# Kernel optimization log

Measured on AMD Instinct MI355X. Metric: run time of the kernel, lower is better.

The kernel has to match this reference:

```python
import jax, jax.numpy as jnp
import numpy as np

B, S, H, D = 4, 2048, 16, 64

def setup_inputs() -> dict:
    key = jax.random.key(0)
    kq, kk, kv = jax.random.split(key, 3)
    q = jax.random.normal(kq, (B, S, H, D), dtype=jnp.float32)
    k = jax.random.normal(kk, (B, S, H, D), dtype=jnp.float32)
    v = jax.random.normal(kv, (B, S, H, D), dtype=jnp.float32)
    return {"q": q, "k": k, "v": v}

def reference(q, k, v):
    # q,k,v: [B,S,H,D]; mask=None path -> additive causal mask; training=False (no dropout)
    batch, seq_len, num_heads, head_dim = q.shape
    scale = head_dim ** -0.5
    qk = jnp.einsum('bqhd,bkhd->bhqk', q, k) * scale  # [B,H,S,S]
    causal = jnp.triu(jnp.ones((seq_len, seq_len), dtype=qk.dtype), k=1)  # 1 above diagonal
    qk = qk + causal[None, None] * jnp.asarray(-1e9, dtype=qk.dtype)
    attn = jax.nn.softmax(qk, axis=-1)
    out = jnp.einsum('bhqk,bkhd->bqhd', attn, v)  # [B,S,H,D]
    return out
```

## Files before the change

### kernel.cpp

```cpp
#include <hip/hip_runtime.h>

#define S_  2048
#define H_  16
#define D_  64
#define HD_ (H_ * D_)
#define LDP 40

using bf16x8 = __attribute__((ext_vector_type(8))) __bf16;
using bf16x4 = __attribute__((ext_vector_type(4))) __bf16;
using f32x4  = __attribute__((ext_vector_type(4))) float;

__device__ __forceinline__ f32x4 mfma16(bf16x8 a, bf16x8 b, f32x4 c) {
    return __builtin_amdgcn_mfma_f32_16x16x32_bf16(a, b, c, 0, 0, 0);
}

__device__ __forceinline__ void glds16(const void* g, void* l) {
    __builtin_amdgcn_global_load_lds((const __attribute__((address_space(1))) void*)g,
                                     (__attribute__((address_space(3))) void*)l, 16, 0, 0);
}

__global__ __launch_bounds__(256, 4)
void prepack(const float* __restrict__ Kg, const float* __restrict__ Vg,
             __bf16* __restrict__ Kb, __bf16* __restrict__ Vtb) {
    __shared__ __bf16 T[64 * 66];
    const int tid = threadIdx.x;
    const int st  = blockIdx.x;
    const int bh  = blockIdx.y;
    const int b = bh >> 4, h = bh & 15;
    if (blockIdx.z == 0) {
#pragma unroll
        for (int rep = 0; rep < 4; ++rep) {
            int lin = rep * 256 + tid;
            int r  = lin >> 4;
            int dq = (lin & 15) << 2;
            float4 x = *(const float4*)(Kg + ((size_t)(b * S_ + st * 64 + r) * H_ + h) * D_ + dq);
            bf16x4 u = {(__bf16)x.x, (__bf16)x.y, (__bf16)x.z, (__bf16)x.w};
            *(bf16x4*)(Kb + ((size_t)bh * S_ + st * 64 + r) * D_ + dq) = u;
        }
    } else {
#pragma unroll
        for (int rep = 0; rep < 4; ++rep) {
            int lin = rep * 256 + tid;
            int r  = lin >> 4;
            int dq = (lin & 15) << 2;
            float4 x = *(const float4*)(Vg + ((size_t)(b * S_ + st * 64 + r) * H_ + h) * D_ + dq);
            T[r * 66 + dq + 0] = (__bf16)x.x;
            T[r * 66 + dq + 1] = (__bf16)x.y;
            T[r * 66 + dq + 2] = (__bf16)x.z;
            T[r * 66 + dq + 3] = (__bf16)x.w;
        }
        __syncthreads();
#pragma unroll
        for (int rep = 0; rep < 4; ++rep) {
            int lin = rep * 256 + tid;
            int d  = lin >> 4;
            int s4 = (lin & 15) << 2;
            bf16x4 u = {T[(s4 + 0) * 66 + d], T[(s4 + 1) * 66 + d],
                        T[(s4 + 2) * 66 + d], T[(s4 + 3) * 66 + d]};
            *(bf16x4*)(Vtb + ((size_t)bh * D_ + d) * S_ + st * 64 + s4) = u;
        }
    }
}

__global__ __launch_bounds__(256, 4)
void fa_fwd(const float* __restrict__ Qg,
            const __bf16* __restrict__ Kb, const __bf16* __restrict__ Vtb,
            float* __restrict__ Og) {
    __shared__ __align__(16) __bf16 Kbuf[2][2048];
    __shared__ __align__(16) __bf16 Vbuf[2][2048];
    __shared__ __bf16 Ps[2560];

    const int tid  = threadIdx.x;
    const int lane = tid & 63;
    const int wave = tid >> 6;
    const int l16  = lane & 15;
    const int quad = lane >> 4;

    const int p   = blockIdx.x;
    const int tHi = 31 - p;
    const int tLo = p;
    const int bh  = blockIdx.y;
    const int b   = bh >> 4;
    const int h   = bh & 15;

    const float sc = 0.18033688f;

    const int kl = lane >> 3, ksl = lane & 7;
    const __bf16* kdma = Kb + ((size_t)bh * S_ + wave * 8 + kl) * D_ + ((ksl ^ kl) << 3);
    const int dl = lane >> 2, vsl = lane & 3;
    const __bf16* vdma = Vtb + ((size_t)bh * D_ + wave * 16 + dl) * S_ + ((vsl ^ (dl & 3)) << 3);

    glds16(kdma, &Kbuf[0][wave * 512]);
    glds16(vdma, &Vbuf[0][wave * 512]);

    const size_t qbase = (size_t)b * S_ * HD_ + (size_t)h * D_;
    const float* Qp = Qg + qbase;
    float*       Op = Og + qbase;
    bf16x8 qh[2], ql[2];
#pragma unroll
    for (int kf = 0; kf < 2; ++kf) {
        const float* qph = Qp + (size_t)(tHi * 64 + wave * 16 + l16) * HD_ + quad * 8 + kf * 32;
        const float* qpl = Qp + (size_t)(tLo * 64 + wave * 16 + l16) * HD_ + quad * 8 + kf * 32;
        float4 x = *(const float4*)(qph);
        float4 y = *(const float4*)(qph + 4);
        bf16x8 f;
        f[0] = (__bf16)x.x; f[1] = (__bf16)x.y; f[2] = (__bf16)x.z; f[3] = (__bf16)x.w;
        f[4] = (__bf16)y.x; f[5] = (__bf16)y.y; f[6] = (__bf16)y.z; f[7] = (__bf16)y.w;
        qh[kf] = f;
        x = *(const float4*)(qpl);
        y = *(const float4*)(qpl + 4);
        f[0] = (__bf16)x.x; f[1] = (__bf16)x.y; f[2] = (__bf16)x.z; f[3] = (__bf16)x.w;
        f[4] = (__bf16)y.x; f[5] = (__bf16)y.y; f[6] = (__bf16)y.z; f[7] = (__bf16)y.w;
        ql[kf] = f;
    }

    f32x4 oh[4], ol[4];
    float lh[4], ll[4];
#pragma unroll
    for (int nd = 0; nd < 4; ++nd) { oh[nd] = (f32x4)0.f; ol[nd] = (f32x4)0.f; }
#pragma unroll
    for (int r = 0; r < 4; ++r) { lh[r] = 0.f; ll[r] = 0.f; }

    auto process = [&](f32x4* s, bool diag, int dOff, f32x4* oacc, float* lsum, int cb) {
#pragma unroll
        for (int nt = 0; nt < 2; ++nt)
#pragma unroll
            for (int r = 0; r < 4; ++r) {
                float v = s[nt][r] * sc;
                if (diag && (dOff + nt * 16 + l16 > wave * 16 + quad * 4 + r)) v = -1e30f;
                float pe = __builtin_amdgcn_exp2f(v);
                s[nt][r] = pe;
                lsum[r] += pe;
            }
        __bf16* pw = &Ps[(wave * 16 + quad * 4) * LDP + l16];
#pragma unroll
        for (int r = 0; r < 4; ++r)
#pragma unroll
            for (int nt = 0; nt < 2; ++nt)
                pw[r * LDP + nt * 16] = (__bf16)s[nt][r];
        bf16x8 a = *(const bf16x8*)&Ps[(wave * 16 + l16) * LDP + quad * 8];
#pragma unroll
        for (int nd = 0; nd < 4; ++nd) {
            bf16x8 bv = *(const bf16x8*)&Vbuf[cb][(nd * 16 + l16) * 32 + ((quad ^ (l16 & 3)) << 3)];
            oacc[nd] = mfma16(a, bv, oacc[nd]);
        }
    };

    const int nkt = 64 - 2 * p;
    __syncthreads();
    for (int kt = 0; kt < nkt; ++kt) {
        const int cb = kt & 1;
        if (kt + 1 < nkt) {
            glds16(kdma + (size_t)(kt + 1) * 2048, &Kbuf[cb ^ 1][wave * 512]);
            glds16(vdma + (kt + 1) * 32,           &Vbuf[cb ^ 1][wave * 512]);
        }
        const bool loAct = (kt < 2 * p + 2);
        f32x4 sh[2], sl[2];
#pragma unroll
        for (int nt = 0; nt < 2; ++nt) { sh[nt] = (f32x4)0.f; sl[nt] = (f32x4)0.f; }
#pragma unroll
        for (int nt = 0; nt < 2; ++nt)
#pragma unroll
            for (int kf = 0; kf < 2; ++kf) {
                bf16x8 bk = *(const bf16x8*)&Kbuf[cb][(nt * 16 + l16) * 64 +
                                 ((((kf << 2) + quad) ^ (l16 & 7)) << 3)];
                sh[nt] = mfma16(qh[kf], bk, sh[nt]);
                if (loAct) sl[nt] = mfma16(ql[kf], bk, sl[nt]);
            }
        process(sh, kt >= 2 * tHi, kt * 32 - tHi * 64, oh, lh, cb);
        if (loAct) process(sl, kt >= 2 * tLo, kt * 32 - tLo * 64, ol, ll, cb);
        __syncthreads();
    }

    auto finish = [&](f32x4* oacc, float* lsum, int trow) {
#pragma unroll
        for (int r = 0; r < 4; ++r) {
            float s = lsum[r];
            s += __shfl_xor(s, 1);
            s += __shfl_xor(s, 2);
            s += __shfl_xor(s, 4);
            s += __shfl_xor(s, 8);
            float inv = 1.0f / s;
            float* op = Op + (size_t)(trow * 64 + wave * 16 + quad * 4 + r) * HD_;
#pragma unroll
            for (int nd = 0; nd < 4; ++nd)
                op[nd * 16 + l16] = oacc[nd][r] * inv;
        }
    };
    finish(oh, lh, tHi);
    finish(ol, ll, tLo);
}

#define LDAF 66
#define LDPF 68
__global__ __launch_bounds__(256, 4)
void fa_fwd_fb(const float* __restrict__ Qg, const float* __restrict__ Kg,
               const float* __restrict__ Vg, float* __restrict__ Og) {
    __shared__ __bf16 Ks[64 * LDAF];
    __shared__ __bf16 Vt[64 * LDAF];
    __shared__ __bf16 Ps[4 * 16 * LDPF];
    const int tid = threadIdx.x, lane = tid & 63, wave = tid >> 6;
    const int l16 = lane & 15, quad = lane >> 4;
    const int p = blockIdx.x, tHi = 31 - p, tLo = p;
    const int bh = blockIdx.y, b = bh >> 4, h = bh & 15;
    const float sc = 0.18033688f;
    const size_t base = (size_t)b * S_ * HD_ + (size_t)h * D_;
    const float* Qp = Qg + base; const float* Kp = Kg + base;
    const float* Vp = Vg + base; float* Op = Og + base;
    bf16x8 qh[2], ql[2];
#pragma unroll
    for (int kf = 0; kf < 2; ++kf) {
        const float* qph = Qp + (size_t)(tHi * 64 + wave * 16 + l16) * HD_ + quad * 8 + kf * 32;
        const float* qpl = Qp + (size_t)(tLo * 64 + wave * 16 + l16) * HD_ + quad * 8 + kf * 32;
        float4 x = *(const float4*)(qph); float4 y = *(const float4*)(qph + 4);
        bf16x8 f;
        f[0]=(__bf16)x.x; f[1]=(__bf16)x.y; f[2]=(__bf16)x.z; f[3]=(__bf16)x.w;
        f[4]=(__bf16)y.x; f[5]=(__bf16)y.y; f[6]=(__bf16)y.z; f[7]=(__bf16)y.w;
        qh[kf] = f;
        x = *(const float4*)(qpl); y = *(const float4*)(qpl + 4);
        f[0]=(__bf16)x.x; f[1]=(__bf16)x.y; f[2]=(__bf16)x.z; f[3]=(__bf16)x.w;
        f[4]=(__bf16)y.x; f[5]=(__bf16)y.y; f[6]=(__bf16)y.z; f[7]=(__bf16)y.w;
        ql[kf] = f;
    }
    f32x4 oh[4], ol[4]; float lh[4], ll[4];
#pragma unroll
    for (int nd = 0; nd < 4; ++nd) { oh[nd] = (f32x4)0.f; ol[nd] = (f32x4)0.f; }
#pragma unroll
    for (int r = 0; r < 4; ++r) { lh[r] = 0.f; ll[r] = 0.f; }
    auto process = [&](f32x4* s, bool diag, f32x4* oacc, float* lsum) {
#pragma unroll
        for (int nt = 0; nt < 4; ++nt)
#pragma unroll
            for (int r = 0; r < 4; ++r) {
                float v = s[nt][r] * sc;
                if (diag && (nt * 16 + l16 > wave * 16 + quad * 4 + r)) v = -1e30f;
                float pe = __builtin_amdgcn_exp2f(v);
                s[nt][r] = pe; lsum[r] += pe;
            }
        __bf16* pw = &Ps[(wave * 16 + quad * 4) * LDPF + l16];
#pragma unroll
        for (int r = 0; r < 4; ++r)
#pragma unroll
            for (int nt = 0; nt < 4; ++nt) pw[r * LDPF + nt * 16] = (__bf16)s[nt][r];
        const __bf16* pr = &Ps[wave * 16 * LDPF];
#pragma unroll
        for (int kf = 0; kf < 2; ++kf) {
            bf16x8 a = *(const bf16x8*)&pr[l16 * LDPF + kf * 32 + quad * 8];
#pragma unroll
            for (int nd = 0; nd < 4; ++nd) {
                bf16x8 bv = *(const bf16x8*)&Vt[(nd * 16 + l16) * LDAF + kf * 32 + quad * 8];
                oacc[nd] = mfma16(a, bv, oacc[nd]);
            }
        }
    };
    const int nkt = 32 - p;
    for (int kt = 0; kt < nkt; ++kt) {
        __syncthreads();
#pragma unroll
        for (int rep = 0; rep < 4; ++rep) {
            int linear = rep * 256 + tid;
            int key = linear >> 4; int dq = (linear & 15) << 2;
            const float* kp = Kp + (size_t)(kt * 64 + key) * HD_ + dq;
            const float* vp = Vp + (size_t)(kt * 64 + key) * HD_ + dq;
            float4 kv = *(const float4*)kp; float4 vv = *(const float4*)vp;
            __bf16* kd = &Ks[key * LDAF + dq];
            kd[0]=(__bf16)kv.x; kd[1]=(__bf16)kv.y; kd[2]=(__bf16)kv.z; kd[3]=(__bf16)kv.w;
            Vt[(dq+0)*LDAF+key]=(__bf16)vv.x; Vt[(dq+1)*LDAF+key]=(__bf16)vv.y;
            Vt[(dq+2)*LDAF+key]=(__bf16)vv.z; Vt[(dq+3)*LDAF+key]=(__bf16)vv.w;
        }
        __syncthreads();
        const bool loAct = (kt <= p);
        f32x4 sh[4], sl[4];
#pragma unroll
        for (int nt = 0; nt < 4; ++nt) { sh[nt] = (f32x4)0.f; sl[nt] = (f32x4)0.f; }
#pragma unroll
        for (int nt = 0; nt < 4; ++nt)
#pragma unroll
            for (int kf = 0; kf < 2; ++kf) {
                bf16x8 bf = *(const bf16x8*)&Ks[(nt * 16 + l16) * LDAF + kf * 32 + quad * 8];
                sh[nt] = mfma16(qh[kf], bf, sh[nt]);
                if (loAct) sl[nt] = mfma16(ql[kf], bf, sl[nt]);
            }
        process(sh, kt == tHi, oh, lh);
        if (loAct) process(sl, kt == tLo, ol, ll);
    }
    auto finish = [&](f32x4* oacc, float* lsum, int trow) {
#pragma unroll
        for (int r = 0; r < 4; ++r) {
            float s = lsum[r];
            s += __shfl_xor(s, 1); s += __shfl_xor(s, 2);
            s += __shfl_xor(s, 4); s += __shfl_xor(s, 8);
            float inv = 1.0f / s;
            float* op = Op + (size_t)(trow * 64 + wave * 16 + quad * 4 + r) * HD_;
#pragma unroll
            for (int nd = 0; nd < 4; ++nd) op[nd * 16 + l16] = oacc[nd][r] * inv;
        }
    };
    finish(oh, lh, tHi); finish(ol, ll, tLo);
}

extern "C" void kernel_launch(void* const* d_in, const int* in_sizes, int n_in,
                              void* d_out, int out_size, void* d_ws, size_t ws_size,
                              hipStream_t stream) {
    const float* q = (const float*)d_in[0];
    const float* k = (const float*)d_in[1];
    const float* v = (const float*)d_in[2];
    float*       o = (float*)d_out;
    const size_t NEL  = (size_t)4 * H_ * S_ * D_;
    const size_t NEED = 2 * NEL * sizeof(__bf16);
    if (ws_size >= NEED) {
        __bf16* Kb  = (__bf16*)d_ws;
        __bf16* Vtb = Kb + NEL;
        dim3 pgrid(S_ / 64, 4 * H_, 2);
        prepack<<<pgrid, 256, 0, stream>>>(k, v, Kb, Vtb);
        dim3 grid(16, 4 * H_);
        fa_fwd<<<grid, 256, 0, stream>>>(q, Kb, Vtb, o);
    } else {
        dim3 grid(16, 4 * H_);
        fa_fwd_fb<<<grid, 256, 0, stream>>>(q, k, v, o);
    }
}
```

Baseline: 207.3 us.

## Widen key tiles to 64, fold scale into K, compute row sums via MFMA

The main kernel now processes 64-key tiles instead of 32, which halves the number of loop iterations and barriers. Each iteration issues two async LDS loads per buffer per wave, and the P staging buffer uses an XOR-swizzled layout in place of padding. The softmax scale is folded into the bf16 K prepack, so the per-element multiply is dropped, and row sums are computed with an MFMA against a ones vector instead of VALU adds and cross-lane shuffles. The cost is more LDS per block (about 40KB), which may lower occupancy below the launch-bound target. Rounding also changes slightly because the scale is applied before the bf16 cast and the row sums come from bf16 P.

```diff
diff --git a/kernel.cpp b/kernel.cpp
--- a/kernel.cpp
+++ b/kernel.cpp
@@ -4,7 +4,7 @@
 #define H_  16
 #define D_  64
 #define HD_ (H_ * D_)
-#define LDP 40
+#define SC_ 0.18033688f
 
 using bf16x8 = __attribute__((ext_vector_type(8))) __bf16;
 using bf16x4 = __attribute__((ext_vector_type(4))) __bf16;
@@ -34,7 +34,8 @@
             int r  = lin >> 4;
             int dq = (lin & 15) << 2;
             float4 x = *(const float4*)(Kg + ((size_t)(b * S_ + st * 64 + r) * H_ + h) * D_ + dq);
-            bf16x4 u = {(__bf16)x.x, (__bf16)x.y, (__bf16)x.z, (__bf16)x.w};
+            bf16x4 u = {(__bf16)(x.x * SC_), (__bf16)(x.y * SC_),
+                        (__bf16)(x.z * SC_), (__bf16)(x.w * SC_)};
             *(bf16x4*)(Kb + ((size_t)bh * S_ + st * 64 + r) * D_ + dq) = u;
         }
     } else {
@@ -66,15 +67,18 @@
 void fa_fwd(const float* __restrict__ Qg,
             const __bf16* __restrict__ Kb, const __bf16* __restrict__ Vtb,
             float* __restrict__ Og) {
-    __shared__ __align__(16) __bf16 Kbuf[2][2048];
-    __shared__ __align__(16) __bf16 Vbuf[2][2048];
-    __shared__ __bf16 Ps[2560];
+    __shared__ __align__(16) __bf16 Kbuf[2][4096];
+    __shared__ __align__(16) __bf16 Vbuf[2][4096];
+    __shared__ __align__(16) __bf16 Ps[4096];
 
     const int tid  = threadIdx.x;
     const int lane = tid & 63;
     const int wave = tid >> 6;
     const int l16  = lane & 15;
     const int quad = lane >> 4;
+    const int l8   = lane & 7;
+    const int lh3  = lane >> 3;
+    const int sw   = l16 & 7;
 
     const int p   = blockIdx.x;
     const int tHi = 31 - p;
@@ -83,15 +87,13 @@
     const int b   = bh >> 4;
     const int h   = bh & 15;
 
-    const float sc = 0.18033688f;
-
-    const int kl = lane >> 3, ksl = lane & 7;
-    const __bf16* kdma = Kb + ((size_t)bh * S_ + wave * 8 + kl) * D_ + ((ksl ^ kl) << 3);
-    const int dl = lane >> 2, vsl = lane & 3;
-    const __bf16* vdma = Vtb + ((size_t)bh * D_ + wave * 16 + dl) * S_ + ((vsl ^ (dl & 3)) << 3);
-
-    glds16(kdma, &Kbuf[0][wave * 512]);
-    glds16(vdma, &Vbuf[0][wave * 512]);
+    const __bf16* kdma = Kb  + ((size_t)bh * S_ + wave * 16 + lh3) * D_ + ((l8 ^ lh3) << 3);
+    const __bf16* vdma = Vtb + ((size_t)bh * D_ + wave * 16 + lh3) * S_ + ((l8 ^ lh3) << 3);
+
+    glds16(kdma,          &Kbuf[0][wave * 1024]);
+    glds16(kdma + 8 * D_, &Kbuf[0][wave * 1024 + 512]);
+    glds16(vdma,          &Vbuf[0][wave * 1024]);
+    glds16(vdma + 8 * S_, &Vbuf[0][wave * 1024 + 512]);
 
     const size_t qbase = (size_t)b * S_ * HD_ + (size_t)h * D_;
     const float* Qp = Qg + qbase;
@@ -114,73 +116,89 @@
         ql[kf] = f;
     }
 
-    f32x4 oh[4], ol[4];
-    float lh[4], ll[4];
+    bf16x8 ones;
+#pragma unroll
+    for (int j = 0; j < 8; ++j) ones[j] = (__bf16)1.0f;
+
+    f32x4 oh[4], ol[4], lh, ll;
 #pragma unroll
     for (int nd = 0; nd < 4; ++nd) { oh[nd] = (f32x4)0.f; ol[nd] = (f32x4)0.f; }
-#pragma unroll
-    for (int r = 0; r < 4; ++r) { lh[r] = 0.f; ll[r] = 0.f; }
-
-    auto process = [&](f32x4* s, bool diag, int dOff, f32x4* oacc, float* lsum, int cb) {
-#pragma unroll
-        for (int nt = 0; nt < 2; ++nt)
-#pragma unroll
-            for (int r = 0; r < 4; ++r) {
-                float v = s[nt][r] * sc;
-                if (diag && (dOff + nt * 16 + l16 > wave * 16 + quad * 4 + r)) v = -1e30f;
-                float pe = __builtin_amdgcn_exp2f(v);
-                s[nt][r] = pe;
-                lsum[r] += pe;
-            }
-        __bf16* pw = &Ps[(wave * 16 + quad * 4) * LDP + l16];
-#pragma unroll
-        for (int r = 0; r < 4; ++r)
-#pragma unroll
-            for (int nt = 0; nt < 2; ++nt)
-                pw[r * LDP + nt * 16] = (__bf16)s[nt][r];
-        bf16x8 a = *(const bf16x8*)&Ps[(wave * 16 + l16) * LDP + quad * 8];
+    lh = (f32x4)0.f; ll = (f32x4)0.f;
+
+    auto process = [&](f32x4* s, bool diag, f32x4* oacc, f32x4& lacc, int cb) {
+        if (diag) {
+#pragma unroll
+            for (int nt = 0; nt < 4; ++nt)
+#pragma unroll
+                for (int r = 0; r < 4; ++r)
+                    if (nt * 16 + l16 > wave * 16 + quad * 4 + r) s[nt][r] = -1e30f;
+        }
+#pragma unroll
+        for (int nt = 0; nt < 4; ++nt)
+#pragma unroll
+            for (int r = 0; r < 4; ++r)
+                s[nt][r] = __builtin_amdgcn_exp2f(s[nt][r]);
+        const int row0 = wave * 16 + quad * 4;
+        const int ch   = l16 >> 3;
+        const int e    = l16 & 7;
+#pragma unroll
+        for (int r = 0; r < 4; ++r) {
+            const int rw = (row0 + r) & 7;
+            __bf16* pw = &Ps[(row0 + r) * 64 + e];
+#pragma unroll
+            for (int nt = 0; nt < 4; ++nt)
+                pw[((nt * 2 + ch) ^ rw) << 3] = (__bf16)s[nt][r];
+        }
+        const __bf16* pr = &Ps[(wave * 16 + l16) * 64];
+        bf16x8 a0 = *(const bf16x8*)&pr[((0 + quad) ^ sw) << 3];
+        bf16x8 a1 = *(const bf16x8*)&pr[((4 + quad) ^ sw) << 3];
 #pragma unroll
         for (int nd = 0; nd < 4; ++nd) {
-            bf16x8 bv = *(const bf16x8*)&Vbuf[cb][(nd * 16 + l16) * 32 + ((quad ^ (l16 & 3)) << 3)];
-            oacc[nd] = mfma16(a, bv, oacc[nd]);
-        }
+            const __bf16* vr = &Vbuf[cb][(nd * 16 + l16) * 64];
+            bf16x8 bv0 = *(const bf16x8*)&vr[((0 + quad) ^ sw) << 3];
+            bf16x8 bv1 = *(const bf16x8*)&vr[((4 + quad) ^ sw) << 3];
+            oacc[nd] = mfma16(a0, bv0, oacc[nd]);
+            oacc[nd] = mfma16(a1, bv1, oacc[nd]);
+        }
+        lacc = mfma16(a0, ones, lacc);
+        lacc = mfma16(a1, ones, lacc);
     };
 
-    const int nkt = 64 - 2 * p;
+    const int nkt = 32 - p;
     __syncthreads();
     for (int kt = 0; kt < nkt; ++kt) {
         const int cb = kt & 1;
         if (kt + 1 < nkt) {
-            glds16(kdma + (size_t)(kt + 1) * 2048, &Kbuf[cb ^ 1][wave * 512]);
-            glds16(vdma + (kt + 1) * 32,           &Vbuf[cb ^ 1][wave * 512]);
-        }
-        const bool loAct = (kt < 2 * p + 2);
-        f32x4 sh[2], sl[2];
-#pragma unroll
-        for (int nt = 0; nt < 2; ++nt) { sh[nt] = (f32x4)0.f; sl[nt] = (f32x4)0.f; }
-#pragma unroll
-        for (int nt = 0; nt < 2; ++nt)
+            const __bf16* kp = kdma + (size_t)(kt + 1) * 4096;
+            const __bf16* vp = vdma + (kt + 1) * 64;
+            glds16(kp,          &Kbuf[cb ^ 1][wave * 1024]);
+            glds16(kp + 8 * D_, &Kbuf[cb ^ 1][wave * 1024 + 512]);
+            glds16(vp,          &Vbuf[cb ^ 1][wave * 1024]);
+            glds16(vp + 8 * S_, &Vbuf[cb ^ 1][wave * 1024 + 512]);
+        }
+        const bool loAct = (kt <= p);
+        f32x4 sh[4], sl[4];
+#pragma unroll
+        for (int nt = 0; nt < 4; ++nt) { sh[nt] = (f32x4)0.f; sl[nt] = (f32x4)0.f; }
+#pragma unroll
+        for (int nt = 0; nt < 4; ++nt) {
+            const __bf16* kr = &Kbuf[cb][(nt * 16 + l16) * 64];
 #pragma unroll
             for (int kf = 0; kf < 2; ++kf) {
-                bf16x8 bk = *(const bf16x8*)&Kbuf[cb][(nt * 16 + l16) * 64 +
-                                 ((((kf << 2) + quad) ^ (l16 & 7)) << 3)];
+                bf16x8 bk = *(const bf16x8*)&kr[(((kf << 2) + quad) ^ sw) << 3];
                 sh[nt] = mfma16(qh[kf], bk, sh[nt]);
                 if (loAct) sl[nt] = mfma16(ql[kf], bk, sl[nt]);
             }
-        process(sh, kt >= 2 * tHi, kt * 32 - tHi * 64, oh, lh, cb);
-        if (loAct) process(sl, kt >= 2 * tLo, kt * 32 - tLo * 64, ol, ll, cb);
+        }
+        process(sh, kt == tHi, oh, lh, cb);
+        if (loAct) process(sl, kt == tLo, ol, ll, cb);
         __syncthreads();
     }
 
-    auto finish = [&](f32x4* oacc, float* lsum, int trow) {
+    auto finish = [&](f32x4* oacc, f32x4& lacc, int trow) {
 #pragma unroll
         for (int r = 0; r < 4; ++r) {
-            float s = lsum[r];
-            s += __shfl_xor(s, 1);
-            s += __shfl_xor(s, 2);
-            s += __shfl_xor(s, 4);
-            s += __shfl_xor(s, 8);
-            float inv = 1.0f / s;
+            float inv = 1.0f / lacc[r];
             float* op = Op + (size_t)(trow * 64 + wave * 16 + quad * 4 + r) * HD_;
 #pragma unroll
             for (int nd = 0; nd < 4; ++nd)
@@ -198,12 +216,11 @@
                const float* __restrict__ Vg, float* __restrict__ Og) {
     __shared__ __bf16 Ks[64 * LDAF];
     __shared__ __bf16 Vt[64 * LDAF];
-    __shared__ __bf16 Ps[4 * 16 * LDPF];
+    __shared__ __bf16 Psf[4 * 16 * LDPF];
     const int tid = threadIdx.x, lane = tid & 63, wave = tid >> 6;
     const int l16 = lane & 15, quad = lane >> 4;
     const int p = blockIdx.x, tHi = 31 - p, tLo = p;
     const int bh = blockIdx.y, b = bh >> 4, h = bh & 15;
-    const float sc = 0.18033688f;
     const size_t base = (size_t)b * S_ * HD_ + (size_t)h * D_;
     const float* Qp = Qg + base; const float* Kp = Kg + base;
     const float* Vp = Vg + base; float* Op = Og + base;
@@ -232,17 +249,17 @@
         for (int nt = 0; nt < 4; ++nt)
 #pragma unroll
             for (int r = 0; r < 4; ++r) {
-                float v = s[nt][r] * sc;
+                float v = s[nt][r] * SC_;
                 if (diag && (nt * 16 + l16 > wave * 16 + quad * 4 + r)) v = -1e30f;
                 float pe = __builtin_amdgcn_exp2f(v);
                 s[nt][r] = pe; lsum[r] += pe;
             }
-        __bf16* pw = &Ps[(wave * 16 + quad * 4) * LDPF + l16];
+        __bf16* pw = &Psf[(wave * 16 + quad * 4) * LDPF + l16];
 #pragma unroll
         for (int r = 0; r < 4; ++r)
 #pragma unroll
             for (int nt = 0; nt < 4; ++nt) pw[r * LDPF + nt * 16] = (__bf16)s[nt][r];
-        const __bf16* pr = &Ps[wave * 16 * LDPF];
+        const __bf16* pr = &Psf[wave * 16 * LDPF];
 #pragma unroll
         for (int kf = 0; kf < 2; ++kf) {
             bf16x8 a = *(const bf16x8*)&pr[l16 * LDPF + kf * 32 + quad * 8];
```

Measured after the change: 337.0 us. 62.6% more time.

## Fold softmax scale into K prepack, compute row sums via MFMA, remap grid

Applied to the files above, without the earlier changes.

The softmax scale is applied to K during bf16 prepacking, which removes the per-score multiply in the inner loop. Row sums are now accumulated with an extra MFMA against a ones vector instead of scalar adds plus a cross-lane shuffle reduction. The grid is flattened to 1D with a block-to-(bh, p) mapping meant to spread work across CUs. The trade-offs are an extra MFMA per tile, row sums taken from the bf16-rounded probabilities, and an extra rounding step on the pre-scaled K.

```diff
diff --git a/kernel.cpp b/kernel.cpp
--- a/kernel.cpp
+++ b/kernel.cpp
@@ -4,6 +4,7 @@
 #define H_  16
 #define D_  64
 #define HD_ (H_ * D_)
+#define SC_ 0.18033688f
 #define LDP 40
 
 using bf16x8 = __attribute__((ext_vector_type(8))) __bf16;
@@ -34,7 +35,8 @@
             int r  = lin >> 4;
             int dq = (lin & 15) << 2;
             float4 x = *(const float4*)(Kg + ((size_t)(b * S_ + st * 64 + r) * H_ + h) * D_ + dq);
-            bf16x4 u = {(__bf16)x.x, (__bf16)x.y, (__bf16)x.z, (__bf16)x.w};
+            bf16x4 u = {(__bf16)(x.x * SC_), (__bf16)(x.y * SC_),
+                        (__bf16)(x.z * SC_), (__bf16)(x.w * SC_)};
             *(bf16x4*)(Kb + ((size_t)bh * S_ + st * 64 + r) * D_ + dq) = u;
         }
     } else {
@@ -68,7 +70,7 @@
             float* __restrict__ Og) {
     __shared__ __align__(16) __bf16 Kbuf[2][2048];
     __shared__ __align__(16) __bf16 Vbuf[2][2048];
-    __shared__ __bf16 Ps[2560];
+    __shared__ __align__(16) __bf16 Ps[2560];
 
     const int tid  = threadIdx.x;
     const int lane = tid & 63;
@@ -76,14 +78,13 @@
     const int l16  = lane & 15;
     const int quad = lane >> 4;
 
-    const int p   = blockIdx.x;
+    const int lin = blockIdx.x;
+    const int bh  = (lin & 7) + ((lin >> 3) & 7) * 8;
+    const int p   = lin >> 6;
     const int tHi = 31 - p;
     const int tLo = p;
-    const int bh  = blockIdx.y;
     const int b   = bh >> 4;
     const int h   = bh & 15;
-
-    const float sc = 0.18033688f;
 
     const int kl = lane >> 3, ksl = lane & 7;
     const __bf16* kdma = Kb + ((size_t)bh * S_ + wave * 8 + kl) * D_ + ((ksl ^ kl) << 3);
@@ -114,24 +115,28 @@
         ql[kf] = f;
     }
 
-    f32x4 oh[4], ol[4];
-    float lh[4], ll[4];
+    bf16x8 ones;
+#pragma unroll
+    for (int j = 0; j < 8; ++j) ones[j] = (__bf16)1.0f;
+
+    f32x4 oh[4], ol[4], lh, ll;
 #pragma unroll
     for (int nd = 0; nd < 4; ++nd) { oh[nd] = (f32x4)0.f; ol[nd] = (f32x4)0.f; }
-#pragma unroll
-    for (int r = 0; r < 4; ++r) { lh[r] = 0.f; ll[r] = 0.f; }
-
-    auto process = [&](f32x4* s, bool diag, int dOff, f32x4* oacc, float* lsum, int cb) {
+    lh = (f32x4)0.f; ll = (f32x4)0.f;
+
+    auto process = [&](f32x4* s, bool diag, int dOff, f32x4* oacc, f32x4& lacc, int cb) {
+        if (diag) {
+#pragma unroll
+            for (int nt = 0; nt < 2; ++nt)
+#pragma unroll
+                for (int r = 0; r < 4; ++r)
+                    if (dOff + nt * 16 + l16 > wave * 16 + quad * 4 + r) s[nt][r] = -1e30f;
+        }
 #pragma unroll
         for (int nt = 0; nt < 2; ++nt)
 #pragma unroll
-            for (int r = 0; r < 4; ++r) {
-                float v = s[nt][r] * sc;
-                if (diag && (dOff + nt * 16 + l16 > wave * 16 + quad * 4 + r)) v = -1e30f;
-                float pe = __builtin_amdgcn_exp2f(v);
-                s[nt][r] = pe;
-                lsum[r] += pe;
-            }
+            for (int r = 0; r < 4; ++r)
+                s[nt][r] = __builtin_amdgcn_exp2f(s[nt][r]);
         __bf16* pw = &Ps[(wave * 16 + quad * 4) * LDP + l16];
 #pragma unroll
         for (int r = 0; r < 4; ++r)
@@ -144,6 +149,7 @@
             bf16x8 bv = *(const bf16x8*)&Vbuf[cb][(nd * 16 + l16) * 32 + ((quad ^ (l16 & 3)) << 3)];
             oacc[nd] = mfma16(a, bv, oacc[nd]);
         }
+        lacc = mfma16(a, ones, lacc);
     };
 
     const int nkt = 64 - 2 * p;
@@ -172,15 +178,10 @@
         __syncthreads();
     }
 
-    auto finish = [&](f32x4* oacc, float* lsum, int trow) {
+    auto finish = [&](f32x4* oacc, f32x4& lacc, int trow) {
 #pragma unroll
         for (int r = 0; r < 4; ++r) {
-            float s = lsum[r];
-            s += __shfl_xor(s, 1);
-            s += __shfl_xor(s, 2);
-            s += __shfl_xor(s, 4);
-            s += __shfl_xor(s, 8);
-            float inv = 1.0f / s;
+            float inv = 1.0f / lacc[r];
             float* op = Op + (size_t)(trow * 64 + wave * 16 + quad * 4 + r) * HD_;
 #pragma unroll
             for (int nd = 0; nd < 4; ++nd)
@@ -198,12 +199,11 @@
                const float* __restrict__ Vg, float* __restrict__ Og) {
     __shared__ __bf16 Ks[64 * LDAF];
     __shared__ __bf16 Vt[64 * LDAF];
-    __shared__ __bf16 Ps[4 * 16 * LDPF];
+    __shared__ __bf16 Psf[4 * 16 * LDPF];
     const int tid = threadIdx.x, lane = tid & 63, wave = tid >> 6;
     const int l16 = lane & 15, quad = lane >> 4;
-    const int p = blockIdx.x, tHi = 31 - p, tLo = p;
-    const int bh = blockIdx.y, b = bh >> 4, h = bh & 15;
-    const float sc = 0.18033688f;
+    const int p = blockIdx.x & 15, tHi = 31 - p, tLo = p;
+    const int bh = blockIdx.x >> 4, b = bh >> 4, h = bh & 15;
     const size_t base = (size_t)b * S_ * HD_ + (size_t)h * D_;
     const float* Qp = Qg + base; const float* Kp = Kg + base;
     const float* Vp = Vg + base; float* Op = Og + base;
@@ -232,17 +232,17 @@
         for (int nt = 0; nt < 4; ++nt)
 #pragma unroll
             for (int r = 0; r < 4; ++r) {
-                float v = s[nt][r] * sc;
+                float v = s[nt][r] * SC_;
                 if (diag && (nt * 16 + l16 > wave * 16 + quad * 4 + r)) v = -1e30f;
                 float pe = __builtin_amdgcn_exp2f(v);
                 s[nt][r] = pe; lsum[r] += pe;
             }
-        __bf16* pw = &Ps[(wave * 16 + quad * 4) * LDPF + l16];
+        __bf16* pw = &Psf[(wave * 16 + quad * 4) * LDPF + l16];
 #pragma unroll
         for (int r = 0; r < 4; ++r)
 #pragma unroll
             for (int nt = 0; nt < 4; ++nt) pw[r * LDPF + nt * 16] = (__bf16)s[nt][r];
-        const __bf16* pr = &Ps[wave * 16 * LDPF];
+        const __bf16* pr = &Psf[wave * 16 * LDPF];
 #pragma unroll
         for (int kf = 0; kf < 2; ++kf) {
             bf16x8 a = *(const bf16x8*)&pr[l16 * LDPF + kf * 32 + quad * 8];
@@ -313,10 +313,8 @@
         __bf16* Vtb = Kb + NEL;
         dim3 pgrid(S_ / 64, 4 * H_, 2);
         prepack<<<pgrid, 256, 0, stream>>>(k, v, Kb, Vtb);
-        dim3 grid(16, 4 * H_);
-        fa_fwd<<<grid, 256, 0, stream>>>(q, Kb, Vtb, o);
+        fa_fwd<<<dim3(1024), 256, 0, stream>>>(q, Kb, Vtb, o);
     } else {
-        dim3 grid(16, 4 * H_);
-        fa_fwd_fb<<<grid, 256, 0, stream>>>(q, k, v, o);
-    }
-}
+        fa_fwd_fb<<<dim3(1024), 256, 0, stream>>>(q, k, v, o);
+    }
+}
```

After: 190.1 us. 8.3% less time.
